# Optimization experiments

Hardware: AMD Instinct MI355X
Metric: run time of the kernel (lower is better)

Reference implementation:

```python
import jax, jax.numpy as jnp
import numpy as np
import math

H = 768      # hidden_size
NH = 12      # num_head
DH = H // NH # head dim
FF = 4 * H
EPS = 1e-6

def _layernorm(x, g, b):
    mu = jnp.mean(x, axis=-1, keepdims=True)
    var = jnp.mean(jnp.square(x - mu), axis=-1, keepdims=True)
    return (x - mu) * jax.lax.rsqrt(var + EPS) * g + b

def setup_inputs() -> dict:
    key = jax.random.key(0)
    ks = jax.random.split(key, 16)
    B, N = 8, 1024
    xav = lambda k, i, o: jax.random.uniform(k, (i, o), jnp.float32, -1.0, 1.0) * math.sqrt(6.0 / (i + o))
    bias = lambda k, o: jax.random.normal(k, (o,), jnp.float32) * 1e-6
    return {
        "x": jax.random.normal(ks[0], (B, N, H), jnp.float32),
        "wq": xav(ks[1], H, H), "bq": bias(ks[2], H),
        "wk": xav(ks[3], H, H), "bk": bias(ks[4], H),
        "wv": xav(ks[5], H, H), "bv": bias(ks[6], H),
        "wo": xav(ks[7], H, H), "bo": bias(ks[8], H),
        "w1": xav(ks[9], H, FF), "b1": bias(ks[10], FF),
        "w2": xav(ks[11], FF, H), "b2": bias(ks[12], H),
        "g1": jnp.ones((H,), jnp.float32), "be1": jnp.zeros((H,), jnp.float32),
        "g2": jnp.ones((H,), jnp.float32), "be2": jnp.zeros((H,), jnp.float32),
    }

def reference(x, wq, bq, wk, bk, wv, bv, wo, bo, w1, b1, w2, b2, g1, be1, g2, be2):
    B, N, _ = x.shape
    x1 = _layernorm(x, g1, be1)
    # QKV projections -> (B, NH, N, DH)
    split = lambda t: t.reshape(B, N, NH, DH).transpose(0, 2, 1, 3)
    q = split(x1 @ wq + bq)
    k = split(x1 @ wk + bk)
    v = split(x1 @ wv + bv)
    # NOTE: original divides by sqrt(attention_size)=sqrt(H), not sqrt(DH)
    scores = jnp.einsum("bhqd,bhkd->bhqk", q, k) / math.sqrt(H)
    weights = jax.nn.softmax(scores, axis=-1)
    ctx = jnp.einsum("bhqk,bhkd->bhqd", weights, v)
    ctx = ctx.transpose(0, 2, 1, 3).reshape(B, N, H)
    attn_out = ctx @ wo + bo  # dropout is identity in eval
    x = x + attn_out
    x2 = _layernorm(x, g2, be2)
    h = jax.nn.gelu(x2 @ w1 + b1, approximate=False)  # torch F.gelu is exact erf gelu
    mlp_out = h @ w2 + b2
    x = x + mlp_out
    return (x, weights)
```

## Files before the change

kernel.cpp:

```cpp
#include <hip/hip_runtime.h>
#include <cstdint>
#include <cstddef>

#define H 768
#define NHEAD 12
#define DH 64
#define FFD 3072
#define BATCH 8
#define SEQ 1024
#define NTOK (BATCH*SEQ)

typedef __bf16 bf16x8 __attribute__((ext_vector_type(8)));
typedef float  floatx4 __attribute__((ext_vector_type(4)));

#define MFMA_BF16(a,b,c) __builtin_amdgcn_mfma_f32_16x16x32_bf16((a),(b),(c),0,0,0)

__global__ __launch_bounds__(256) void ln_kernel(const float* __restrict__ x,
                                                 const float* __restrict__ g,
                                                 const float* __restrict__ be,
                                                 __bf16* __restrict__ out) {
    int row  = blockIdx.x * 4 + (threadIdx.x >> 6);
    int lane = threadIdx.x & 63;
    const float* xr = x + (size_t)row * H;
    float v[12];
    float s = 0.f;
#pragma unroll
    for (int i = 0; i < 12; i++) { v[i] = xr[lane + i * 64]; s += v[i]; }
#pragma unroll
    for (int m = 32; m >= 1; m >>= 1) s += __shfl_xor(s, m, 64);
    float mu = s * (1.0f / H);
    float q = 0.f;
#pragma unroll
    for (int i = 0; i < 12; i++) { float d = v[i] - mu; q += d * d; }
#pragma unroll
    for (int m = 32; m >= 1; m >>= 1) q += __shfl_xor(q, m, 64);
    float rstd = rsqrtf(q * (1.0f / H) + 1e-6f);
    __bf16* orow = out + (size_t)row * H;
#pragma unroll
    for (int i = 0; i < 12; i++) {
        int c = lane + i * 64;
        orow[c] = (__bf16)((v[i] - mu) * rstd * g[c] + be[c]);
    }
}

__global__ __launch_bounds__(256) void wtrans_kernel(const float* __restrict__ W,
                                                     __bf16* __restrict__ T,
                                                     int K, int Nn) {
    __shared__ float tile[32][33];
    int tx = threadIdx.x & 31;
    int ty = threadIdx.x >> 5;
    int n0 = blockIdx.x * 32, k0 = blockIdx.y * 32;
#pragma unroll
    for (int i = 0; i < 32; i += 8)
        tile[ty + i][tx] = W[(size_t)(k0 + ty + i) * Nn + n0 + tx];
    __syncthreads();
#pragma unroll
    for (int i = 0; i < 32; i += 8)
        T[(size_t)(n0 + ty + i) * K + k0 + tx] = (__bf16)tile[tx][ty + i];
}

__global__ __launch_bounds__(256) void vtrans_kernel(const __bf16* __restrict__ v,
                                                     __bf16* __restrict__ vT) {
    __shared__ __bf16 tile[64][65];
    int b = blockIdx.z, h = blockIdx.y, n0 = blockIdx.x * 64;
    int tx = threadIdx.x, ty = threadIdx.y;
#pragma unroll
    for (int r = ty; r < 64; r += 4)
        tile[r][tx] = v[((size_t)b * SEQ + n0 + r) * H + h * DH + tx];
    __syncthreads();
#pragma unroll
    for (int c = ty; c < 64; c += 4)
        vT[(((size_t)b * NHEAD + h) * DH + c) * SEQ + n0 + tx] = tile[tx][c];
}

template<bool GELU, bool HAS_RES, bool OUT_BF16>
__global__ __launch_bounds__(256) void gemm_kernel(const __bf16* __restrict__ A,
                                                   const __bf16* __restrict__ Bt,
                                                   const float* __restrict__ bias,
                                                   const float* __restrict__ res,
                                                   __bf16* __restrict__ obf,
                                                   float* __restrict__ ofp,
                                                   int Nn, int K) {
    __shared__ __bf16 As[128 * 32];
    __shared__ __bf16 Bs[128 * 32];
    int tid = threadIdx.x;
    int wave = tid >> 6, lane = tid & 63;
    int wr = wave >> 1, wc = wave & 1;
    int l15 = lane & 15, quad = lane >> 4;

    floatx4 acc[4][4];
    floatx4 zero = {0.f, 0.f, 0.f, 0.f};
#pragma unroll
    for (int i = 0; i < 4; i++)
#pragma unroll
        for (int j = 0; j < 4; j++) acc[i][j] = zero;

    int srow = tid >> 1;
    int scol = (tid & 1) * 16;
    const __bf16* Ag = A + (size_t)(blockIdx.y * 128 + srow) * K + scol;
    const __bf16* Bg = Bt + (size_t)(blockIdx.x * 128 + srow) * K + scol;
    __bf16* AsW = &As[srow * 32 + scol];
    __bf16* BsW = &Bs[srow * 32 + scol];

    for (int k0 = 0; k0 < K; k0 += 32) {
        *(bf16x8*)(AsW)     = *(const bf16x8*)(Ag + k0);
        *(bf16x8*)(AsW + 8) = *(const bf16x8*)(Ag + k0 + 8);
        *(bf16x8*)(BsW)     = *(const bf16x8*)(Bg + k0);
        *(bf16x8*)(BsW + 8) = *(const bf16x8*)(Bg + k0 + 8);
        __syncthreads();
        bf16x8 af[4], bfv[4];
#pragma unroll
        for (int i = 0; i < 4; i++)
            af[i] = *(const bf16x8*)&As[(wr * 64 + i * 16 + l15) * 32 + quad * 8];
#pragma unroll
        for (int j = 0; j < 4; j++)
            bfv[j] = *(const bf16x8*)&Bs[(wc * 64 + j * 16 + l15) * 32 + quad * 8];
#pragma unroll
        for (int i = 0; i < 4; i++)
#pragma unroll
            for (int j = 0; j < 4; j++)
                acc[i][j] = MFMA_BF16(af[i], bfv[j], acc[i][j]);
        __syncthreads();
    }

#pragma unroll
    for (int i = 0; i < 4; i++) {
        int row = blockIdx.y * 128 + wr * 64 + i * 16 + quad * 4;
#pragma unroll
        for (int j = 0; j < 4; j++) {
            int col = blockIdx.x * 128 + wc * 64 + j * 16 + l15;
            float bsv = bias[col];
#pragma unroll
            for (int r = 0; r < 4; r++) {
                float vv = acc[i][j][r] + bsv;
                if (GELU) vv = 0.5f * vv * (1.0f + erff(vv * 0.70710678118654752f));
                if (HAS_RES) vv += res[(size_t)(row + r) * Nn + col];
                if (OUT_BF16) obf[(size_t)(row + r) * Nn + col] = (__bf16)vv;
                else          ofp[(size_t)(row + r) * Nn + col] = vv;
            }
        }
    }
}


__device__ __forceinline__ int sbidx(int row, int col) {
    return row * 1024 + (col ^ ((row & 7) << 3));
}

__global__ __launch_bounds__(256, 4) void attn_kernel(const __bf16* __restrict__ q,
                                                      const __bf16* __restrict__ k,
                                                      const __bf16* __restrict__ vT,
                                                      float* __restrict__ Wout,
                                                      __bf16* __restrict__ ctx) {
    __shared__ __bf16 Sb[16 * 1024];
    __shared__ __align__(16) float red[2][16][4];
    int tid = threadIdx.x;
    int wave = tid >> 6, lane = tid & 63, l15 = lane & 15, quad = lane >> 4;
    int rt = blockIdx.x, h = blockIdx.y, b = blockIdx.z;
    const size_t qkbase = ((size_t)b * SEQ) * H + h * DH;
    const float scale = 0.03608439182435161f;

    const __bf16* qrow = q + qkbase + (size_t)(rt * 16 + l15) * H;
    bf16x8 qf0 = *(const bf16x8*)(qrow + quad * 8);
    bf16x8 qf1 = *(const bf16x8*)(qrow + 32 + quad * 8);

    floatx4 s[16];
    const __bf16* kbase = k + qkbase;
#pragma unroll
    for (int i = 0; i < 16; i++) {
        int ct = wave * 16 + i;
        const __bf16* krow = kbase + (size_t)(ct * 16 + l15) * H;
        bf16x8 kf0 = *(const bf16x8*)(krow + quad * 8);
        bf16x8 kf1 = *(const bf16x8*)(krow + 32 + quad * 8);
        floatx4 a = {0.f, 0.f, 0.f, 0.f};
        a = MFMA_BF16(qf0, kf0, a);
        a = MFMA_BF16(qf1, kf1, a);
#pragma unroll
        for (int r = 0; r < 4; r++) s[i][r] = a[r] * scale;
    }

    float m4[4];
#pragma unroll
    for (int r = 0; r < 4; r++) {
        float m = s[0][r];
#pragma unroll
        for (int i = 1; i < 16; i++) m = fmaxf(m, s[i][r]);
#pragma unroll
        for (int msk = 8; msk >= 1; msk >>= 1) m = fmaxf(m, __shfl_xor(m, msk, 64));
        m4[r] = m;
    }
    if (l15 == 0) {
#pragma unroll
        for (int r = 0; r < 4; r++) red[0][quad * 4 + r][wave] = m4[r];
    }
    __syncthreads();
    float mrow[4];
#pragma unroll
    for (int r = 0; r < 4; r++) {
        float4 rr = *(const float4*)&red[0][quad * 4 + r][0];
        mrow[r] = fmaxf(fmaxf(rr.x, rr.y), fmaxf(rr.z, rr.w));
    }

    float s4[4] = {0.f, 0.f, 0.f, 0.f};
#pragma unroll
    for (int i = 0; i < 16; i++) {
#pragma unroll
        for (int r = 0; r < 4; r++) {
            float e = __expf(s[i][r] - mrow[r]);
            s[i][r] = e;
            s4[r] += e;
        }
    }
#pragma unroll
    for (int r = 0; r < 4; r++) {
#pragma unroll
        for (int msk = 8; msk >= 1; msk >>= 1) s4[r] += __shfl_xor(s4[r], msk, 64);
    }
    if (l15 == 0) {
#pragma unroll
        for (int r = 0; r < 4; r++) red[1][quad * 4 + r][wave] = s4[r];
    }
    __syncthreads();
    float inv[4];
#pragma unroll
    for (int r = 0; r < 4; r++) {
        float4 rr = *(const float4*)&red[1][quad * 4 + r][0];
        inv[r] = 1.0f / (rr.x + rr.y + rr.z + rr.w);
    }

    size_t wbase = (((size_t)b * NHEAD + h) * SEQ + rt * 16) * SEQ;
#pragma unroll
    for (int i = 0; i < 16; i++) {
        int col = (wave * 16 + i) * 16 + l15;
#pragma unroll
        for (int r = 0; r < 4; r++) {
            float w = s[i][r] * inv[r];
            int row = quad * 4 + r;
            __builtin_nontemporal_store(w, &Wout[wbase + (size_t)row * SEQ + col]);
            Sb[sbidx(row, col)] = (__bf16)w;
        }
    }
    __syncthreads();

    floatx4 acc = {0.f, 0.f, 0.f, 0.f};
    const __bf16* vbase = vT + (((size_t)b * NHEAD + h) * DH + wave * 16 + l15) * SEQ;
#pragma unroll
    for (int c = 0; c < 32; c++) {
        int k0 = c * 32 + quad * 8;
        bf16x8 af = *(const bf16x8*)&Sb[sbidx(l15, k0)];
        bf16x8 bv = *(const bf16x8*)(vbase + k0);
        acc = MFMA_BF16(af, bv, acc);
    }
#pragma unroll
    for (int r = 0; r < 4; r++)
        ctx[((size_t)b * SEQ + rt * 16 + quad * 4 + r) * H + h * DH + wave * 16 + l15] =
            (__bf16)acc[r];
}

extern "C" void kernel_launch(void* const* d_in, const int* in_sizes, int n_in,
                              void* d_out, int out_size, void* d_ws, size_t ws_size,
                              hipStream_t stream) {
    const float* x   = (const float*)d_in[0];
    const float* wq  = (const float*)d_in[1];
    const float* bq  = (const float*)d_in[2];
    const float* wk  = (const float*)d_in[3];
    const float* bk  = (const float*)d_in[4];
    const float* wv  = (const float*)d_in[5];
    const float* bv  = (const float*)d_in[6];
    const float* wo  = (const float*)d_in[7];
    const float* bo  = (const float*)d_in[8];
    const float* w1  = (const float*)d_in[9];
    const float* b1  = (const float*)d_in[10];
    const float* w2  = (const float*)d_in[11];
    const float* b2  = (const float*)d_in[12];
    const float* g1  = (const float*)d_in[13];
    const float* be1 = (const float*)d_in[14];
    const float* g2  = (const float*)d_in[15];
    const float* be2 = (const float*)d_in[16];

    char* ws = (char*)d_ws;
    const size_t SZB = (size_t)NTOK * H * 2;
    __bf16* x1b  = (__bf16*)(ws);
    __bf16* qb   = (__bf16*)(ws + SZB);
    __bf16* kb   = (__bf16*)(ws + 2 * SZB);
    __bf16* vb   = (__bf16*)(ws + 3 * SZB);
    __bf16* vTb  = (__bf16*)(ws + 4 * SZB);
    __bf16* ctxb = (__bf16*)(ws + 5 * SZB);
    __bf16* x2b  = (__bf16*)(ws + 6 * SZB);
    __bf16* hb   = (__bf16*)(ws + 7 * SZB);
    size_t off = 7 * SZB + (size_t)NTOK * FFD * 2;
    float* xattn = (float*)(ws + off); off += (size_t)NTOK * H * 4;
    __bf16* wqT = (__bf16*)(ws + off); off += (size_t)H * H * 2;
    __bf16* wkT = (__bf16*)(ws + off); off += (size_t)H * H * 2;
    __bf16* wvT = (__bf16*)(ws + off); off += (size_t)H * H * 2;
    __bf16* woT = (__bf16*)(ws + off); off += (size_t)H * H * 2;
    __bf16* w1T = (__bf16*)(ws + off); off += (size_t)H * FFD * 2;
    __bf16* w2T = (__bf16*)(ws + off); off += (size_t)FFD * H * 2;

    float* outx = (float*)d_out;
    float* outw = (float*)d_out + (size_t)NTOK * H;

    wtrans_kernel<<<dim3(24, 24), 256, 0, stream>>>(wq, wqT, H, H);
    wtrans_kernel<<<dim3(24, 24), 256, 0, stream>>>(wk, wkT, H, H);
    wtrans_kernel<<<dim3(24, 24), 256, 0, stream>>>(wv, wvT, H, H);
    wtrans_kernel<<<dim3(24, 24), 256, 0, stream>>>(wo, woT, H, H);
    wtrans_kernel<<<dim3(96, 24), 256, 0, stream>>>(w1, w1T, H, FFD);
    wtrans_kernel<<<dim3(24, 96), 256, 0, stream>>>(w2, w2T, FFD, H);

    ln_kernel<<<NTOK / 4, 256, 0, stream>>>(x, g1, be1, x1b);

    gemm_kernel<false, false, true><<<dim3(H / 128, NTOK / 128), 256, 0, stream>>>(
        x1b, wqT, bq, nullptr, qb, nullptr, H, H);
    gemm_kernel<false, false, true><<<dim3(H / 128, NTOK / 128), 256, 0, stream>>>(
        x1b, wkT, bk, nullptr, kb, nullptr, H, H);
    gemm_kernel<false, false, true><<<dim3(H / 128, NTOK / 128), 256, 0, stream>>>(
        x1b, wvT, bv, nullptr, vb, nullptr, H, H);

    vtrans_kernel<<<dim3(16, NHEAD, BATCH), dim3(64, 4), 0, stream>>>(vb, vTb);

    attn_kernel<<<dim3(64, NHEAD, BATCH), 256, 0, stream>>>(qb, kb, vTb, outw, ctxb);

    gemm_kernel<false, true, false><<<dim3(H / 128, NTOK / 128), 256, 0, stream>>>(
        ctxb, woT, bo, x, nullptr, xattn, H, H);

    ln_kernel<<<NTOK / 4, 256, 0, stream>>>(xattn, g2, be2, x2b);

    gemm_kernel<true, false, true><<<dim3(FFD / 128, NTOK / 128), 256, 0, stream>>>(
        x2b, w1T, b1, nullptr, hb, nullptr, FFD, H);

    gemm_kernel<false, true, false><<<dim3(H / 128, NTOK / 128), 256, 0, stream>>>(
        hb, w2T, b2, xattn, nullptr, outx, H, FFD);
}
```

Baseline: 898.6 us.

## Fuse QKV projections into one GEMM and use direct global-to-LDS loads

```diff
diff --git a/kernel.cpp b/kernel.cpp
--- a/kernel.cpp
+++ b/kernel.cpp
@@ -9,11 +9,18 @@
 #define BATCH 8
 #define SEQ 1024
 #define NTOK (BATCH*SEQ)
+#define QKVS 2304
 
 typedef __bf16 bf16x8 __attribute__((ext_vector_type(8)));
 typedef float  floatx4 __attribute__((ext_vector_type(4)));
 
 #define MFMA_BF16(a,b,c) __builtin_amdgcn_mfma_f32_16x16x32_bf16((a),(b),(c),0,0,0)
+
+__device__ __forceinline__ void gload16(const void* g, void* l) {
+    __builtin_amdgcn_global_load_lds((const __attribute__((address_space(1))) void*)g,
+                                     (__attribute__((address_space(3))) void*)l,
+                                     16, 0, 0);
+}
 
 __global__ __launch_bounds__(256) void ln_kernel(const float* __restrict__ x,
                                                  const float* __restrict__ g,
@@ -59,14 +66,25 @@
         T[(size_t)(n0 + ty + i) * K + k0 + tx] = (__bf16)tile[tx][ty + i];
 }
 
-__global__ __launch_bounds__(256) void vtrans_kernel(const __bf16* __restrict__ v,
+__global__ __launch_bounds__(256) void bcat_kernel(const float* __restrict__ bq,
+                                                   const float* __restrict__ bk,
+                                                   const float* __restrict__ bv,
+                                                   float* __restrict__ o) {
+    int i = blockIdx.x * 256 + threadIdx.x;
+    if (i >= 3 * H) return;
+    if (i < H) o[i] = bq[i];
+    else if (i < 2 * H) o[i] = bk[i - H];
+    else o[i] = bv[i - 2 * H];
+}
+
+__global__ __launch_bounds__(256) void vtrans_kernel(const __bf16* __restrict__ qkv,
                                                      __bf16* __restrict__ vT) {
     __shared__ __bf16 tile[64][65];
     int b = blockIdx.z, h = blockIdx.y, n0 = blockIdx.x * 64;
     int tx = threadIdx.x, ty = threadIdx.y;
 #pragma unroll
     for (int r = ty; r < 64; r += 4)
-        tile[r][tx] = v[((size_t)b * SEQ + n0 + r) * H + h * DH + tx];
+        tile[r][tx] = qkv[((size_t)b * SEQ + n0 + r) * QKVS + 2 * H + h * DH + tx];
     __syncthreads();
 #pragma unroll
     for (int c = ty; c < 64; c += 4)
@@ -95,18 +113,22 @@
 #pragma unroll
         for (int j = 0; j < 4; j++) acc[i][j] = zero;
 
-    int srow = tid >> 1;
-    int scol = (tid & 1) * 16;
-    const __bf16* Ag = A + (size_t)(blockIdx.y * 128 + srow) * K + scol;
-    const __bf16* Bg = Bt + (size_t)(blockIdx.x * 128 + srow) * K + scol;
-    __bf16* AsW = &As[srow * 32 + scol];
-    __bf16* BsW = &Bs[srow * 32 + scol];
+    int c0 = wave * 2, c1 = c0 + 1;
+    int lr = lane >> 2, lc = (lane & 3) * 8;
+    const __bf16* Ag0 = A + (size_t)(blockIdx.y * 128 + c0 * 16 + lr) * K + lc;
+    const __bf16* Ag1 = A + (size_t)(blockIdx.y * 128 + c1 * 16 + lr) * K + lc;
+    const __bf16* Bg0 = Bt + (size_t)(blockIdx.x * 128 + c0 * 16 + lr) * K + lc;
+    const __bf16* Bg1 = Bt + (size_t)(blockIdx.x * 128 + c1 * 16 + lr) * K + lc;
+    __bf16* AsD0 = &As[c0 * 512];
+    __bf16* AsD1 = &As[c1 * 512];
+    __bf16* BsD0 = &Bs[c0 * 512];
+    __bf16* BsD1 = &Bs[c1 * 512];
 
     for (int k0 = 0; k0 < K; k0 += 32) {
-        *(bf16x8*)(AsW)     = *(const bf16x8*)(Ag + k0);
-        *(bf16x8*)(AsW + 8) = *(const bf16x8*)(Ag + k0 + 8);
-        *(bf16x8*)(BsW)     = *(const bf16x8*)(Bg + k0);
-        *(bf16x8*)(BsW + 8) = *(const bf16x8*)(Bg + k0 + 8);
+        gload16(Ag0 + k0, AsD0);
+        gload16(Ag1 + k0, AsD1);
+        gload16(Bg0 + k0, BsD0);
+        gload16(Bg1 + k0, BsD1);
         __syncthreads();
         bf16x8 af[4], bfv[4];
 #pragma unroll
@@ -142,13 +164,11 @@
     }
 }
 
-
 __device__ __forceinline__ int sbidx(int row, int col) {
     return row * 1024 + (col ^ ((row & 7) << 3));
 }
 
-__global__ __launch_bounds__(256, 4) void attn_kernel(const __bf16* __restrict__ q,
-                                                      const __bf16* __restrict__ k,
+__global__ __launch_bounds__(256, 4) void attn_kernel(const __bf16* __restrict__ qkv,
                                                       const __bf16* __restrict__ vT,
                                                       float* __restrict__ Wout,
                                                       __bf16* __restrict__ ctx) {
@@ -157,19 +177,19 @@
     int tid = threadIdx.x;
     int wave = tid >> 6, lane = tid & 63, l15 = lane & 15, quad = lane >> 4;
     int rt = blockIdx.x, h = blockIdx.y, b = blockIdx.z;
-    const size_t qkbase = ((size_t)b * SEQ) * H + h * DH;
+    const size_t tokbase = (size_t)b * SEQ * QKVS + h * DH;
     const float scale = 0.03608439182435161f;
 
-    const __bf16* qrow = q + qkbase + (size_t)(rt * 16 + l15) * H;
+    const __bf16* qrow = qkv + tokbase + (size_t)(rt * 16 + l15) * QKVS;
     bf16x8 qf0 = *(const bf16x8*)(qrow + quad * 8);
     bf16x8 qf1 = *(const bf16x8*)(qrow + 32 + quad * 8);
 
     floatx4 s[16];
-    const __bf16* kbase = k + qkbase;
+    const __bf16* kbase = qkv + tokbase + H;
 #pragma unroll
     for (int i = 0; i < 16; i++) {
         int ct = wave * 16 + i;
-        const __bf16* krow = kbase + (size_t)(ct * 16 + l15) * H;
+        const __bf16* krow = kbase + (size_t)(ct * 16 + l15) * QKVS;
         bf16x8 kf0 = *(const bf16x8*)(krow + quad * 8);
         bf16x8 kf1 = *(const bf16x8*)(krow + 32 + quad * 8);
         floatx4 a = {0.f, 0.f, 0.f, 0.f};
@@ -281,44 +301,38 @@
     char* ws = (char*)d_ws;
     const size_t SZB = (size_t)NTOK * H * 2;
     __bf16* x1b  = (__bf16*)(ws);
-    __bf16* qb   = (__bf16*)(ws + SZB);
-    __bf16* kb   = (__bf16*)(ws + 2 * SZB);
-    __bf16* vb   = (__bf16*)(ws + 3 * SZB);
+    __bf16* qkvb = (__bf16*)(ws + SZB);
     __bf16* vTb  = (__bf16*)(ws + 4 * SZB);
     __bf16* ctxb = (__bf16*)(ws + 5 * SZB);
     __bf16* x2b  = (__bf16*)(ws + 6 * SZB);
     __bf16* hb   = (__bf16*)(ws + 7 * SZB);
     size_t off = 7 * SZB + (size_t)NTOK * FFD * 2;
     float* xattn = (float*)(ws + off); off += (size_t)NTOK * H * 4;
-    __bf16* wqT = (__bf16*)(ws + off); off += (size_t)H * H * 2;
-    __bf16* wkT = (__bf16*)(ws + off); off += (size_t)H * H * 2;
-    __bf16* wvT = (__bf16*)(ws + off); off += (size_t)H * H * 2;
-    __bf16* woT = (__bf16*)(ws + off); off += (size_t)H * H * 2;
-    __bf16* w1T = (__bf16*)(ws + off); off += (size_t)H * FFD * 2;
-    __bf16* w2T = (__bf16*)(ws + off); off += (size_t)FFD * H * 2;
+    __bf16* wqkvT = (__bf16*)(ws + off); off += (size_t)3 * H * H * 2;
+    __bf16* woT  = (__bf16*)(ws + off); off += (size_t)H * H * 2;
+    __bf16* w1T  = (__bf16*)(ws + off); off += (size_t)H * FFD * 2;
+    __bf16* w2T  = (__bf16*)(ws + off); off += (size_t)FFD * H * 2;
+    float* bqkv  = (float*)(ws + off); off += (size_t)3 * H * 4;
 
     float* outx = (float*)d_out;
     float* outw = (float*)d_out + (size_t)NTOK * H;
 
-    wtrans_kernel<<<dim3(24, 24), 256, 0, stream>>>(wq, wqT, H, H);
-    wtrans_kernel<<<dim3(24, 24), 256, 0, stream>>>(wk, wkT, H, H);
-    wtrans_kernel<<<dim3(24, 24), 256, 0, stream>>>(wv, wvT, H, H);
+    wtrans_kernel<<<dim3(24, 24), 256, 0, stream>>>(wq, wqkvT, H, H);
+    wtrans_kernel<<<dim3(24, 24), 256, 0, stream>>>(wk, wqkvT + (size_t)H * H, H, H);
+    wtrans_kernel<<<dim3(24, 24), 256, 0, stream>>>(wv, wqkvT + (size_t)2 * H * H, H, H);
     wtrans_kernel<<<dim3(24, 24), 256, 0, stream>>>(wo, woT, H, H);
     wtrans_kernel<<<dim3(96, 24), 256, 0, stream>>>(w1, w1T, H, FFD);
     wtrans_kernel<<<dim3(24, 96), 256, 0, stream>>>(w2, w2T, FFD, H);
+    bcat_kernel<<<9, 256, 0, stream>>>(bq, bk, bv, bqkv);
 
     ln_kernel<<<NTOK / 4, 256, 0, stream>>>(x, g1, be1, x1b);
 
-    gemm_kernel<false, false, true><<<dim3(H / 128, NTOK / 128), 256, 0, stream>>>(
-        x1b, wqT, bq, nullptr, qb, nullptr, H, H);
-    gemm_kernel<false, false, true><<<dim3(H / 128, NTOK / 128), 256, 0, stream>>>(
-        x1b, wkT, bk, nullptr, kb, nullptr, H, H);
-    gemm_kernel<false, false, true><<<dim3(H / 128, NTOK / 128), 256, 0, stream>>>(
-        x1b, wvT, bv, nullptr, vb, nullptr, H, H);
-
-    vtrans_kernel<<<dim3(16, NHEAD, BATCH), dim3(64, 4), 0, stream>>>(vb, vTb);
-
-    attn_kernel<<<dim3(64, NHEAD, BATCH), 256, 0, stream>>>(qb, kb, vTb, outw, ctxb);
+    gemm_kernel<false, false, true><<<dim3(QKVS / 128, NTOK / 128), 256, 0, stream>>>(
+        x1b, wqkvT, bqkv, nullptr, qkvb, nullptr, QKVS, H);
+
+    vtrans_kernel<<<dim3(16, NHEAD, BATCH), dim3(64, 4), 0, stream>>>(qkvb, vTb);
+
+    attn_kernel<<<dim3(64, NHEAD, BATCH), 256, 0, stream>>>(qkvb, vTb, outw, ctxb);
 
     gemm_kernel<false, true, false><<<dim3(H / 128, NTOK / 128), 256, 0, stream>>>(
         ctxb, woT, bo, x, nullptr, xattn, H, H);
```

Result: faster. 864.6 us (-3.8%).
